# Kernel optimization log

Hardware: AMD Instinct MI355X
Metric: run time of the kernel (lower is better)

Reference implementation:

```python
import jax, jax.numpy as jnp
import numpy as np
import math

W = 256           # one-sided sliding window
G = 64            # number of global tokens (first G positions of every batch row)
HEADS = 8
DMID = 512
HD = DMID // HEADS
B = 2
S = 4096
NEG = jnp.float32(-1e9)   # stands in for the -inf written by mask_invalid_locations (same softmax result)


def setup_inputs() -> dict:
    key = jax.random.key(0)
    ks = jax.random.split(key, 10)
    f = lambda k, sh: jax.random.normal(k, sh, dtype=jnp.float32)
    inp = {
        'hidden_states': f(ks[0], (B, S, DMID)),
        'q': f(ks[1], (S, B, DMID)),
        'k': f(ks[2], (S, B, DMID)),
        'v': f(ks[3], (S, B, DMID)),
        'attn_mask': jnp.broadcast_to((jnp.arange(S) < G).astype(jnp.int32), (B, S)),
    }
    for i, n in enumerate(['q', 'k', 'v', 'qg', 'kg', 'vg']):
        inp['W' + n] = f(ks[4 + i], (DMID, DMID)) * 0.02
        inp['b' + n] = jnp.zeros((DMID,), jnp.float32)
    return inp


def _proj(x, Wt, b):
    # x: (S,B,E) -> (B,S,H,HD)   (matches nn.Linear then view(seq,b,h,hd).transpose(0,1))
    y = x @ Wt.T + b
    return jnp.swapaxes(y.reshape(S, B, HEADS, HD), 0, 1)


def _local_qk(qh, kh):
    # qh, kh: (B,S,H,HD) -> banded scores (B,S,H,2W+1); entry j = key position i + j - W
    C = S // W
    k_pad = jnp.pad(kh, ((0, 0), (W, W), (0, 0), (0, 0)))
    blk = jnp.arange(C)[:, None] * W + jnp.arange(3 * W)[None, :]      # (C,3W) into padded seq
    k_blk = k_pad[:, blk]                                              # (B,C,3W,H,HD)
    q_blk = qh.reshape(B, C, W, HEADS, HD)
    s = jnp.einsum('bcxhd,bcyhd->bcxhy', q_blk, k_blk)                 # (B,C,W,H,3W)
    band = jnp.arange(W)[:, None] + jnp.arange(2 * W + 1)[None, :]     # (W,2W+1): y = x + j
    diag = jnp.take_along_axis(s, band[None, None, :, None, :], axis=-1)
    return diag.reshape(B, S, HEADS, 2 * W + 1)


def _local_pv(p, vh):
    # p: (B,S,H,2W+1) banded probs; vh: (B,S,H,HD) -> (B,S,H,HD)
    C = S // W
    v_pad = jnp.pad(vh, ((0, 0), (W, W), (0, 0), (0, 0)))
    blk = jnp.arange(C)[:, None] * W + jnp.arange(3 * W)[None, :]
    v_blk = v_pad[:, blk]                                              # (B,C,3W,H,HD)
    pc = jnp.moveaxis(p.reshape(B, C, W, HEADS, 2 * W + 1), 3, 2)      # (B,C,H,W,2W+1)
    padded = jnp.pad(pc, ((0, 0), (0, 0), (0, 0), (0, 0), (0, W)))     # (B,C,H,W,3W+1)
    # skew trick: flatten + truncate turns row x shifted by x -> band[x, x+j] = p[x, j]
    full = padded.reshape(B, C, HEADS, W * (3 * W + 1))[..., :W * 3 * W]
    full = full.reshape(B, C, HEADS, W, 3 * W)
    out = jnp.einsum('bchxy,bcyhd->bcxhd', full, v_blk)
    return out.reshape(B, S, HEADS, HD)


def _forward(hidden_states, q, k, v, attn_mask,
             Wq, bq, Wk, bk, Wv, bv, Wqg, bqg, Wkg, bkg, Wvg, bvg):
    scale = 1.0 / math.sqrt(HD)
    qh = _proj(q, Wq, bq) * scale
    kh = _proj(k, Wk, bk)
    vh = _proj(v, Wv, bv)

    local = _local_qk(qh, kh)                                          # (B,S,H,2W+1)
    pos = jnp.arange(S)[:, None] + jnp.arange(2 * W + 1)[None, :] - W  # (S,2W+1) key index
    valid = (pos >= 0) & (pos < S)
    posc = jnp.clip(pos, 0, S - 1)
    # remove_from_windowed_attention_mask: -10000 at nonzero-mask (global/pad) key positions
    fm = jnp.where(attn_mask != 0, jnp.float32(-10000.0), jnp.float32(0.0))  # (B,S)
    dmask = jnp.where(valid[None], fm[:, posc], 0.0)                   # (B,S,2W+1)
    local = jnp.where(valid[None, :, None, :], local, NEG) + dmask[:, :, None, :]

    # every query also attends to the G global keys (concatenated in front)
    sel = jnp.einsum('bshd,bghd->bshg', qh, kh[:, :G])                 # (B,S,H,G)
    scores = jnp.concatenate([sel, local], axis=-1)                    # (B,S,H,G+2W+1)
    probs = jax.nn.softmax(scores, axis=-1)
    kp = attn_mask < 0                                                 # padding queries -> zero rows
    probs = jnp.where(kp[:, :, None, None], 0.0, probs)

    out = jnp.einsum('bshg,bghd->bshd', probs[..., :G], vh[:, :G])
    out = out + _local_pv(probs[..., G:], vh)
    out = out.reshape(B, S, DMID)

    # global-query full attention (W_*_global on hidden_states), overwrites global rows
    qg = ((hidden_states[:, :G] @ Wqg.T + bqg) * scale).reshape(B, G, HEADS, HD)
    kg = (hidden_states @ Wkg.T + bkg).reshape(B, S, HEADS, HD)
    vg = (hidden_states @ Wvg.T + bvg).reshape(B, S, HEADS, HD)
    gw = jnp.einsum('bghd,bshd->bhgs', qg, kg)                         # (B,H,G,S)
    gw = jnp.where(kp[:, None, None, :], jnp.float32(-10000.0), gw)
    gp = jax.nn.softmax(gw, axis=-1)
    gout = jnp.einsum('bhgs,bshd->bghd', gp, vg).reshape(B, G, DMID)
    out = out.at[:, :G, :].set(gout)
    return out


def reference(hidden_states, q, k, v, attn_mask,
              Wq, bq, Wk, bk, Wv, bv, Wqg, bqg, Wkg, bkg, Wvg, bvg):
    return _forward(hidden_states, q, k, v, attn_mask,
                    Wq, bq, Wk, bk, Wv, bv, Wqg, bqg, Wkg, bkg, Wvg, bvg)
```

## Files before the change

### kernel.cpp

```cpp
#include <hip/hip_runtime.h>
#include <cstdint>

#define S_   4096
#define B_   2
#define H_   8
#define HD_  64
#define DM_  512
#define G_   64
#define SEGN 16

typedef __attribute__((ext_vector_type(8))) short bf8_t;
typedef __attribute__((ext_vector_type(4))) float f4_t;
typedef __attribute__((ext_vector_type(4))) unsigned u4_t;
#define MFMA16(A,Bv,C) __builtin_amdgcn_mfma_f32_16x16x32_bf16((A),(Bv),(C),0,0,0)

typedef const unsigned __attribute__((address_space(1)))* gp1_t;
typedef unsigned __attribute__((address_space(3)))* lp3_t;
static __device__ __forceinline__ void gld16(const void* g, void* l){
    __builtin_amdgcn_global_load_lds((gp1_t)g, (lp3_t)l, 16, 0, 0);
}

static __device__ __forceinline__ unsigned short f2bf(float x){
    union { float f; unsigned u; } v; v.f = x;
    unsigned r = v.u + 0x7FFFu + ((v.u >> 16) & 1u);
    return (unsigned short)(r >> 16);
}
static __device__ __forceinline__ unsigned pksplit(float x){
    unsigned u = __float_as_uint(x);
    unsigned t = u & 0xFFFF0000u;
    float r = x - __uint_as_float(t);
    return (u >> 16) | (__float_as_uint(r) & 0xFFFF0000u);
}
static __device__ __forceinline__ float rmax16(float x){
    x=fmaxf(x,__shfl_xor(x,1)); x=fmaxf(x,__shfl_xor(x,2));
    x=fmaxf(x,__shfl_xor(x,4)); x=fmaxf(x,__shfl_xor(x,8)); return x;
}
static __device__ __forceinline__ float rsum16(float x){
    x+=__shfl_xor(x,1); x+=__shfl_xor(x,2); x+=__shfl_xor(x,4); x+=__shfl_xor(x,8); return x;
}

__device__ __forceinline__ int in_row_map(int m, int perm) {
    if (perm == 0) return m;
    if (perm == 1) { int b = m >> 12, s = m & 4095; return s * 2 + b; }
    { int b = m >> 6, g = m & 63; return b * S_ + g; }
}

struct SplitArgs { float* p[4]; };
__global__ __launch_bounds__(256) void split_inplace(SplitArgs a){
    int t = blockIdx.x >> 12;
    int idx = (blockIdx.x & 4095) * 256 + threadIdx.x;
    float* p = a.p[t];
    float4 x = *(const float4*)(p + (size_t)idx * 4);
    unsigned o[4] = { pksplit(x.x), pksplit(x.y), pksplit(x.z), pksplit(x.w) };
    *(u4_t*)(p + (size_t)idx * 4) = *(const u4_t*)o;
}

struct WexpArgs { const float* src[6]; float alpha[6]; unsigned* wa; unsigned* wb; };
__global__ __launch_bounds__(256) void wexpand(WexpArgs a){
    int g = blockIdx.x >> 8;
    int idx = ((blockIdx.x & 255) * 256 + threadIdx.x) * 4;
    const float* s = a.src[g];
    float al = a.alpha[g];
    size_t base = (size_t)g * 262144 + idx;
    float4 x = *(const float4*)(s + idx);
    float xs[4] = { x.x*al, x.y*al, x.z*al, x.w*al };
    unsigned wa4[4], wb4[4];
    #pragma unroll
    for (int j = 0; j < 4; ++j) {
        unsigned u = __float_as_uint(xs[j]);
        unsigned t = u & 0xFFFF0000u;
        float r = xs[j] - __uint_as_float(t);
        unsigned lo = __float_as_uint(r) & 0xFFFF0000u;
        wa4[j] = (u >> 16) | t;
        wb4[j] = (lo >> 16) | lo;
    }
    *(u4_t*)(a.wa + base) = *(const u4_t*)wa4;
    *(u4_t*)(a.wb + base) = *(const u4_t*)wb4;
}

struct ProjDesc {
    const unsigned* A2; const unsigned* Wa; const unsigned* Wb; const float* bias;
    unsigned short* out_r; unsigned short* out_t;
    float balpha; int perm; int mode; int mtiles;
};
struct ProjBatch { ProjDesc d[6]; };

__global__ __launch_bounds__(256) void proj6(ProjBatch pb){
    __shared__ unsigned Asl[128*32];
    __shared__ unsigned Wasl[128*32];
    __shared__ unsigned Wbsl[128*32];
    const ProjDesc d = pb.d[blockIdx.z];
    if ((int)blockIdx.x >= d.mtiles) return;
    const int tid = threadIdx.x;
    const int m0 = blockIdx.x*128, n0 = blockIdx.y*128;
    const int w = tid>>6, l = tid&63, wr = w>>1, wc = w&1, lg = l>>4, lc = l&15;
    const int grow = l>>3, gchk = l&7;

    f4_t acc[4][4];
    #pragma unroll
    for(int i=0;i<4;++i)
        #pragma unroll
        for(int j=0;j<4;++j) acc[i][j] = (f4_t){0.f,0.f,0.f,0.f};

    for (int k0 = 0; k0 < 16; ++k0) {
        __syncthreads();
        #pragma unroll
        for (int t = 0; t < 4; ++t) {
            int row = t*32 + w*8 + grow;
            int sw = (gchk ^ (row & 7)) << 2;
            gld16(d.A2 + (size_t)in_row_map(m0+row, d.perm)*DM_ + k0*32 + sw,
                  (char*)Asl + (t*32 + w*8)*128);
            gld16(d.Wa + (size_t)(n0+row)*DM_ + k0*32 + sw,
                  (char*)Wasl + (t*32 + w*8)*128);
            gld16(d.Wb + (size_t)(n0+row)*DM_ + k0*32 + sw,
                  (char*)Wbsl + (t*32 + w*8)*128);
        }
        __syncthreads();
        #pragma unroll
        for (int ks = 0; ks < 2; ++ks) {
            bf8_t af[4];
            #pragma unroll
            for (int mf = 0; mf < 4; ++mf) {
                int r = wr*64 + mf*16 + lc;
                af[mf] = *(const bf8_t*)((const char*)Asl + r*128 + (((ks*4+lg) ^ (r&7))<<4));
            }
            #pragma unroll
            for (int nf = 0; nf < 4; ++nf) {
                int r = wc*64 + nf*16 + lc;
                int off = r*128 + (((ks*4+lg) ^ (r&7))<<4);
                bf8_t wa = *(const bf8_t*)((const char*)Wasl + off);
                bf8_t wb = *(const bf8_t*)((const char*)Wbsl + off);
                #pragma unroll
                for (int mf = 0; mf < 4; ++mf) {
                    acc[mf][nf] = MFMA16(af[mf], wa, acc[mf][nf]);
                    acc[mf][nf] = MFMA16(af[mf], wb, acc[mf][nf]);
                }
            }
        }
    }
    if (d.mode == 0) {
        #pragma unroll
        for(int nf=0;nf<4;++nf){
            int n = n0 + wc*64 + nf*16 + lc;
            float bv = d.bias[n] * d.balpha;
            #pragma unroll
            for(int mf=0;mf<4;++mf){
                int mb = m0 + wr*64 + mf*16 + lg*4;
                #pragma unroll
                for(int i=0;i<4;++i)
                    d.out_r[(size_t)(mb+i)*DM_ + n] = f2bf(acc[mf][nf][i] + bv);
            }
        }
    } else {
        #pragma unroll
        for(int nf=0;nf<4;++nf){
            int n = n0 + wc*64 + nf*16 + lc;
            int h = n>>6, dl = n&63;
            float bv = d.bias[n];
            #pragma unroll
            for(int mf=0;mf<4;++mf){
                int m = m0 + wr*64 + mf*16 + lg*4;
                int b = m>>12, s = m&4095;
                unsigned short q0=f2bf(acc[mf][nf][0]+bv), q1=f2bf(acc[mf][nf][1]+bv);
                unsigned short q2=f2bf(acc[mf][nf][2]+bv), q3=f2bf(acc[mf][nf][3]+bv);
                unsigned pkw[2] = { (unsigned)q0 | ((unsigned)q1<<16),
                                    (unsigned)q2 | ((unsigned)q3<<16) };
                *(uint2*)(d.out_t + ((size_t)((b*H_+h)*HD_ + dl))*S_ + s) = *(const uint2*)pkw;
            }
        }
    }
}

__global__ __launch_bounds__(256) void attn_fused(
    const unsigned short* __restrict__ Qbf, const unsigned short* __restrict__ Kbf,
    const unsigned short* __restrict__ VT, const unsigned short* __restrict__ QGbf,
    const unsigned short* __restrict__ KGbf, const unsigned short* __restrict__ VGT,
    const int* __restrict__ amask, float* __restrict__ out,
    float* __restrict__ part_m, float* __restrict__ part_l, float* __restrict__ part_o)
{
    __shared__ unsigned short Kls[64*64];
    __shared__ unsigned short Vls[64*64];
    __shared__ unsigned short Ps[64*64];
    const int tid=threadIdx.x, b=blockIdx.z, h=blockIdx.y;
    const int w=tid>>6, l=tid&63, lg=l>>4, lc=l&15;
    const bool is_local = (int)blockIdx.x < 63;
    const int s0 = (blockIdx.x+1)*64;
    const int seg = (int)blockIdx.x - 63;

    const unsigned short* Qsrc = is_local ? (Qbf + ((size_t)(b*S_ + s0 + w*16 + lc))*DM_ + h*HD_)
                                          : (QGbf + ((size_t)(b*G_ + w*16 + lc))*DM_ + h*HD_);
    const unsigned short* Ksrc = is_local ? (Kbf + (size_t)b*S_*DM_ + h*HD_)
                                          : (KGbf + (size_t)b*S_*DM_ + h*HD_);
    const unsigned short* Vsrc = is_local ? (VT + ((size_t)(b*H_+h)*HD_)*S_)
                                          : (VGT + ((size_t)(b*H_+h)*HD_)*S_);

    bf8_t qf[2];
    #pragma unroll
    for(int ks=0;ks<2;++ks) qf[ks] = *(const bf8_t*)(Qsrc + ks*32 + lg*8);

    float m_i[4]={-1e30f,-1e30f,-1e30f,-1e30f}, l_i[4]={0.f,0.f,0.f,0.f};
    f4_t acc_o[4];
    #pragma unroll
    for(int nf=0;nf<4;++nf) acc_o[nf]=(f4_t){0.f,0.f,0.f,0.f};

    const int njc = is_local ? 10 : 4;
    for(int jc=0;jc<njc;++jc){
        const int p0 = is_local ? ((jc==0) ? 0 : (s0-256+(jc-1)*64))
                                : (seg*256 + jc*64);
        if ((unsigned)p0 >= (unsigned)S_) continue;
        {
            const int row0 = w*8 + (l>>3), chk = l&7;
            #pragma unroll
            for (int t = 0; t < 2; ++t) {
                int row = t*32 + row0;
                gld16(Ksrc + (size_t)(p0+row)*DM_ + ((chk ^ (row&7))<<3),
                      (char*)Kls + (t*32 + w*8)*128);
                gld16(Vsrc + (size_t)row*S_ + p0 + ((chk ^ (row&7))<<3),
                      (char*)Vls + (t*32 + w*8)*128);
            }
        }
        __syncthreads();
        f4_t s4[4];
        #pragma unroll
        for(int cf=0;cf<4;++cf) s4[cf]=(f4_t){0.f,0.f,0.f,0.f};
        #pragma unroll
        for(int ks=0;ks<2;++ks)
            #pragma unroll
            for(int cf=0;cf<4;++cf){
                int r = cf*16+lc;
                bf8_t kf = *(const bf8_t*)((const char*)Kls + r*128 + (((ks*4+lg)^(r&7))<<4));
                s4[cf]=MFMA16(qf[ks],kf,s4[cf]);
            }
        if(is_local && jc>0){
            #pragma unroll
            for(int cf=0;cf<4;++cf){
                int p = p0 + cf*16 + lc;
                float madd = (amask[b*S_+p]!=0) ? -10000.f : 0.f;
                #pragma unroll
                for(int i=0;i<4;++i){
                    int rel = p - (s0 + w*16 + lg*4 + i);
                    s4[cf][i] = (rel<-256 || rel>256) ? -1e9f : s4[cf][i]+madd;
                }
            }
        }
        float Pv[4][4];
        #pragma unroll
        for(int i=0;i<4;++i){
            float rm = fmaxf(fmaxf(s4[0][i],s4[1][i]),fmaxf(s4[2][i],s4[3][i]));
            rm = rmax16(rm);
            float mn = fmaxf(m_i[i], rm);
            float rs = 0.f;
            #pragma unroll
            for(int cf=0;cf<4;++cf){ float e=__expf(s4[cf][i]-mn); Pv[cf][i]=e; rs+=e; }
            rs = rsum16(rs);
            float f = __expf(m_i[i]-mn);
            l_i[i] = l_i[i]*f + rs;
            m_i[i] = mn;
            #pragma unroll
            for(int nf=0;nf<4;++nf) acc_o[nf][i]*=f;
        }
        #pragma unroll
        for(int cf=0;cf<4;++cf)
            #pragma unroll
            for(int i=0;i<4;++i){
                int qr = w*16+lg*4+i, p = cf*16+lc;
                Ps[qr*64 + ((((p>>3)^(qr&7))<<3) | (p&7))] = f2bf(Pv[cf][i]);
            }
        __syncthreads();
        #pragma unroll
        for(int ks=0;ks<2;++ks){
            int qr = w*16+lc;
            bf8_t pf = *(const bf8_t*)((const char*)Ps + qr*128 + (((ks*4+lg)^(qr&7))<<4));
            #pragma unroll
            for(int nf=0;nf<4;++nf){
                int dr = nf*16+lc;
                bf8_t vf = *(const bf8_t*)((const char*)Vls + dr*128 + (((ks*4+lg)^(dr&7))<<4));
                acc_o[nf] = MFMA16(pf, vf, acc_o[nf]);
            }
        }
        __syncthreads();
    }
    if (is_local) {
        #pragma unroll
        for(int i=0;i<4;++i){
            float inv = 1.f/l_i[i];
            float* orow = out + ((size_t)(b*S_ + s0 + w*16 + lg*4 + i))*DM_ + h*HD_;
            #pragma unroll
            for(int nf=0;nf<4;++nf) orow[nf*16+lc] = acc_o[nf][i]*inv;
        }
    } else {
        const int pid = (b*H_+h)*SEGN + seg;
        #pragma unroll
        for(int i=0;i<4;++i){
            int qrl = w*16 + lg*4 + i;
            #pragma unroll
            for(int nf=0;nf<4;++nf)
                part_o[(size_t)pid*4096 + qrl*64 + nf*16 + lc] = acc_o[nf][i];
            if(lc==0){
                part_m[pid*64+qrl] = m_i[i];
                part_l[pid*64+qrl] = l_i[i];
            }
        }
    }
}

__global__ __launch_bounds__(256) void global_combine(
    const float* __restrict__ part_m, const float* __restrict__ part_l,
    const float* __restrict__ part_o, float* __restrict__ out)
{
    const int bh = blockIdx.x;
    const int b = bh >> 3, h = bh & 7;
    const int tid = threadIdx.x;
    const int q = tid >> 2, d0 = (tid & 3) * 16;
    float mg = -1e30f;
    for (int s = 0; s < SEGN; ++s)
        mg = fmaxf(mg, part_m[(bh * SEGN + s) * 64 + q]);
    float lsum = 0.f, accv[16] = {};
    for (int s = 0; s < SEGN; ++s) {
        const int pid = bh * SEGN + s;
        float wgt = __expf(part_m[pid * 64 + q] - mg);
        lsum += wgt * part_l[pid * 64 + q];
        const float* op = part_o + (size_t)pid * 4096 + q * 64 + d0;
        #pragma unroll
        for (int t = 0; t < 4; ++t) {
            float tmp[4];
            *(float4*)tmp = *(const float4*)(op + t * 4);
            #pragma unroll
            for (int u = 0; u < 4; ++u) accv[t * 4 + u] += wgt * tmp[u];
        }
    }
    float inv = 1.f / lsum;
    float* orow = out + ((size_t)(b * S_ + q)) * DM_ + h * HD_ + d0;
    #pragma unroll
    for (int t = 0; t < 4; ++t) {
        float o[4];
        #pragma unroll
        for (int u = 0; u < 4; ++u) o[u] = accv[t * 4 + u] * inv;
        *(float4*)(orow + t * 4) = *(const float4*)o;
    }
}

extern "C" void kernel_launch(void* const* d_in, const int* in_sizes, int n_in,
                              void* d_out, int out_size, void* d_ws, size_t ws_size,
                              hipStream_t stream) {
    float* hidden = (float*)d_in[0];
    float* q  = (float*)d_in[1];
    float* k  = (float*)d_in[2];
    float* v  = (float*)d_in[3];
    const int* amask = (const int*)d_in[4];
    const float* Wq  = (const float*)d_in[5];  const float* bq  = (const float*)d_in[6];
    const float* Wk  = (const float*)d_in[7];  const float* bk  = (const float*)d_in[8];
    const float* Wv  = (const float*)d_in[9];  const float* bv  = (const float*)d_in[10];
    const float* Wqg = (const float*)d_in[11]; const float* bqg = (const float*)d_in[12];
    const float* Wkg = (const float*)d_in[13]; const float* bkg = (const float*)d_in[14];
    const float* Wvg = (const float*)d_in[15]; const float* bvg = (const float*)d_in[16];
    float* out = (float*)d_out;

    const size_t NE = (size_t)B_ * S_ * DM_;
    unsigned short* Qbf  = (unsigned short*)d_ws;
    unsigned short* Kbf  = Qbf  + NE;
    unsigned short* VT   = Kbf  + NE;
    unsigned short* KGbf = VT   + NE;
    unsigned short* VGT  = KGbf + NE;
    unsigned short* QGbf = VGT  + NE;
    unsigned* Wa = (unsigned*)(QGbf + (size_t)B_*G_*DM_);
    unsigned* Wb = Wa + 6*262144;
    float* po = (float*)Wa;
    float* pm = (float*)Wb;
    float* pl = pm + B_*H_*SEGN*64;

    dim3 blk(256);
    SplitArgs sa; sa.p[0]=hidden; sa.p[1]=q; sa.p[2]=k; sa.p[3]=v;
    hipLaunchKernelGGL(split_inplace, dim3(4*4096), blk, 0, stream, sa);
    WexpArgs we;
    we.src[0]=Wq; we.src[1]=Wk; we.src[2]=Wv; we.src[3]=Wkg; we.src[4]=Wvg; we.src[5]=Wqg;
    we.alpha[0]=0.125f; we.alpha[1]=1.f; we.alpha[2]=1.f;
    we.alpha[3]=1.f; we.alpha[4]=1.f; we.alpha[5]=0.125f;
    we.wa = Wa; we.wb = Wb;
    hipLaunchKernelGGL(wexpand, dim3(1536), blk, 0, stream, we);

    ProjBatch pp;
    pp.d[0] = { (const unsigned*)q,      Wa + 0*262144, Wb + 0*262144, bq,  Qbf,  nullptr, 0.125f, 1, 0, 64 };
    pp.d[1] = { (const unsigned*)k,      Wa + 1*262144, Wb + 1*262144, bk,  Kbf,  nullptr, 1.0f,   1, 0, 64 };
    pp.d[2] = { (const unsigned*)v,      Wa + 2*262144, Wb + 2*262144, bv,  nullptr, VT,   1.0f,   1, 1, 64 };
    pp.d[3] = { (const unsigned*)hidden, Wa + 3*262144, Wb + 3*262144, bkg, KGbf, nullptr, 1.0f,   0, 0, 64 };
    pp.d[4] = { (const unsigned*)hidden, Wa + 4*262144, Wb + 4*262144, bvg, nullptr, VGT,  1.0f,   0, 1, 64 };
    pp.d[5] = { (const unsigned*)hidden, Wa + 5*262144, Wb + 5*262144, bqg, QGbf, nullptr, 0.125f, 2, 0, 1  };
    hipLaunchKernelGGL(proj6, dim3(64,4,6), blk, 0, stream, pp);

    hipLaunchKernelGGL(attn_fused, dim3(63+SEGN, H_, B_), blk, 0, stream,
                       Qbf, Kbf, VT, QGbf, KGbf, VGT, amask, out, pm, pl, po);

    hipLaunchKernelGGL(global_combine, dim3(B_ * H_), blk, 0, stream, pm, pl, po, out);
}
```

Baseline: 294.8 us.

## Drop weight low-part split, add MFMA priority hints, widen global combine grid

The weight expansion now produces only the high bf16 part of each weight, so the projection GEMM loads one weight tile instead of two and issues half the MFMAs. This removes the hi/lo weight compensation and lowers accuracy of the projections. The change also wraps the MFMA blocks in the projection and attention kernels with s_setprio raises. It splits the global_combine kernel across four times as many blocks, each handling four output elements per thread, to spread the work over more CUs.

```diff
diff --git a/kernel.cpp b/kernel.cpp
--- a/kernel.cpp
+++ b/kernel.cpp
@@ -55,7 +55,7 @@
     *(u4_t*)(p + (size_t)idx * 4) = *(const u4_t*)o;
 }
 
-struct WexpArgs { const float* src[6]; float alpha[6]; unsigned* wa; unsigned* wb; };
+struct WexpArgs { const float* src[6]; float alpha[6]; unsigned* wa; };
 __global__ __launch_bounds__(256) void wexpand(WexpArgs a){
     int g = blockIdx.x >> 8;
     int idx = ((blockIdx.x & 255) * 256 + threadIdx.x) * 4;
@@ -64,22 +64,17 @@
     size_t base = (size_t)g * 262144 + idx;
     float4 x = *(const float4*)(s + idx);
     float xs[4] = { x.x*al, x.y*al, x.z*al, x.w*al };
-    unsigned wa4[4], wb4[4];
+    unsigned wa4[4];
     #pragma unroll
     for (int j = 0; j < 4; ++j) {
         unsigned u = __float_as_uint(xs[j]);
-        unsigned t = u & 0xFFFF0000u;
-        float r = xs[j] - __uint_as_float(t);
-        unsigned lo = __float_as_uint(r) & 0xFFFF0000u;
-        wa4[j] = (u >> 16) | t;
-        wb4[j] = (lo >> 16) | lo;
+        wa4[j] = (u >> 16) | (u & 0xFFFF0000u);
     }
     *(u4_t*)(a.wa + base) = *(const u4_t*)wa4;
-    *(u4_t*)(a.wb + base) = *(const u4_t*)wb4;
 }
 
 struct ProjDesc {
-    const unsigned* A2; const unsigned* Wa; const unsigned* Wb; const float* bias;
+    const unsigned* A2; const unsigned* Wa; const float* bias;
     unsigned short* out_r; unsigned short* out_t;
     float balpha; int perm; int mode; int mtiles;
 };
@@ -88,7 +83,6 @@
 __global__ __launch_bounds__(256) void proj6(ProjBatch pb){
     __shared__ unsigned Asl[128*32];
     __shared__ unsigned Wasl[128*32];
-    __shared__ unsigned Wbsl[128*32];
     const ProjDesc d = pb.d[blockIdx.z];
     if ((int)blockIdx.x >= d.mtiles) return;
     const int tid = threadIdx.x;
@@ -112,13 +106,11 @@
                   (char*)Asl + (t*32 + w*8)*128);
             gld16(d.Wa + (size_t)(n0+row)*DM_ + k0*32 + sw,
                   (char*)Wasl + (t*32 + w*8)*128);
-            gld16(d.Wb + (size_t)(n0+row)*DM_ + k0*32 + sw,
-                  (char*)Wbsl + (t*32 + w*8)*128);
         }
         __syncthreads();
         #pragma unroll
         for (int ks = 0; ks < 2; ++ks) {
-            bf8_t af[4];
+            bf8_t af[4], wf[4];
             #pragma unroll
             for (int mf = 0; mf < 4; ++mf) {
                 int r = wr*64 + mf*16 + lc;
@@ -127,15 +119,15 @@
             #pragma unroll
             for (int nf = 0; nf < 4; ++nf) {
                 int r = wc*64 + nf*16 + lc;
-                int off = r*128 + (((ks*4+lg) ^ (r&7))<<4);
-                bf8_t wa = *(const bf8_t*)((const char*)Wasl + off);
-                bf8_t wb = *(const bf8_t*)((const char*)Wbsl + off);
+                wf[nf] = *(const bf8_t*)((const char*)Wasl + r*128 + (((ks*4+lg) ^ (r&7))<<4));
+            }
+            __builtin_amdgcn_s_setprio(1);
+            #pragma unroll
+            for (int nf = 0; nf < 4; ++nf)
                 #pragma unroll
-                for (int mf = 0; mf < 4; ++mf) {
-                    acc[mf][nf] = MFMA16(af[mf], wa, acc[mf][nf]);
-                    acc[mf][nf] = MFMA16(af[mf], wb, acc[mf][nf]);
-                }
-            }
+                for (int mf = 0; mf < 4; ++mf)
+                    acc[mf][nf] = MFMA16(af[mf], wf[nf], acc[mf][nf]);
+            __builtin_amdgcn_s_setprio(0);
         }
     }
     if (d.mode == 0) {
@@ -223,6 +215,7 @@
         f4_t s4[4];
         #pragma unroll
         for(int cf=0;cf<4;++cf) s4[cf]=(f4_t){0.f,0.f,0.f,0.f};
+        __builtin_amdgcn_s_setprio(1);
         #pragma unroll
         for(int ks=0;ks<2;++ks)
             #pragma unroll
@@ -231,6 +224,7 @@
                 bf8_t kf = *(const bf8_t*)((const char*)Kls + r*128 + (((ks*4+lg)^(r&7))<<4));
                 s4[cf]=MFMA16(qf[ks],kf,s4[cf]);
             }
+        __builtin_amdgcn_s_setprio(0);
         if(is_local && jc>0){
             #pragma unroll
             for(int cf=0;cf<4;++cf){
@@ -267,6 +261,7 @@
                 Ps[qr*64 + ((((p>>3)^(qr&7))<<3) | (p&7))] = f2bf(Pv[cf][i]);
             }
         __syncthreads();
+        __builtin_amdgcn_s_setprio(1);
         #pragma unroll
         for(int ks=0;ks<2;++ks){
             int qr = w*16+lc;
@@ -278,6 +273,7 @@
                 acc_o[nf] = MFMA16(pf, vf, acc_o[nf]);
             }
         }
+        __builtin_amdgcn_s_setprio(0);
         __syncthreads();
     }
     if (is_local) {
@@ -308,36 +304,28 @@
     const float* __restrict__ part_m, const float* __restrict__ part_l,
     const float* __restrict__ part_o, float* __restrict__ out)
 {
-    const int bh = blockIdx.x;
+    const int bh = blockIdx.x >> 2, qq = blockIdx.x & 3;
     const int b = bh >> 3, h = bh & 7;
     const int tid = threadIdx.x;
-    const int q = tid >> 2, d0 = (tid & 3) * 16;
+    const int q = qq * 16 + (tid >> 4), d0 = (tid & 15) * 4;
     float mg = -1e30f;
     for (int s = 0; s < SEGN; ++s)
         mg = fmaxf(mg, part_m[(bh * SEGN + s) * 64 + q]);
-    float lsum = 0.f, accv[16] = {};
+    float lsum = 0.f, accv[4] = {};
     for (int s = 0; s < SEGN; ++s) {
         const int pid = bh * SEGN + s;
         float wgt = __expf(part_m[pid * 64 + q] - mg);
         lsum += wgt * part_l[pid * 64 + q];
-        const float* op = part_o + (size_t)pid * 4096 + q * 64 + d0;
-        #pragma unroll
-        for (int t = 0; t < 4; ++t) {
-            float tmp[4];
-            *(float4*)tmp = *(const float4*)(op + t * 4);
-            #pragma unroll
-            for (int u = 0; u < 4; ++u) accv[t * 4 + u] += wgt * tmp[u];
-        }
+        float tmp[4];
+        *(float4*)tmp = *(const float4*)(part_o + (size_t)pid * 4096 + q * 64 + d0);
+        #pragma unroll
+        for (int u = 0; u < 4; ++u) accv[u] += wgt * tmp[u];
     }
     float inv = 1.f / lsum;
-    float* orow = out + ((size_t)(b * S_ + q)) * DM_ + h * HD_ + d0;
-    #pragma unroll
-    for (int t = 0; t < 4; ++t) {
-        float o[4];
-        #pragma unroll
-        for (int u = 0; u < 4; ++u) o[u] = accv[t * 4 + u] * inv;
-        *(float4*)(orow + t * 4) = *(const float4*)o;
-    }
+    float o[4];
+    #pragma unroll
+    for (int u = 0; u < 4; ++u) o[u] = accv[u] * inv;
+    *(float4*)(out + ((size_t)(b * S_ + q)) * DM_ + h * HD_ + d0) = *(const float4*)o;
 }
 
 extern "C" void kernel_launch(void* const* d_in, const int* in_sizes, int n_in,
@@ -364,9 +352,8 @@
     unsigned short* VGT  = KGbf + NE;
     unsigned short* QGbf = VGT  + NE;
     unsigned* Wa = (unsigned*)(QGbf + (size_t)B_*G_*DM_);
-    unsigned* Wb = Wa + 6*262144;
     float* po = (float*)Wa;
-    float* pm = (float*)Wb;
+    float* pm = (float*)(Wa + 4*262144);
     float* pl = pm + B_*H_*SEGN*64;
 
     dim3 blk(256);
@@ -376,20 +363,20 @@
     we.src[0]=Wq; we.src[1]=Wk; we.src[2]=Wv; we.src[3]=Wkg; we.src[4]=Wvg; we.src[5]=Wqg;
     we.alpha[0]=0.125f; we.alpha[1]=1.f; we.alpha[2]=1.f;
     we.alpha[3]=1.f; we.alpha[4]=1.f; we.alpha[5]=0.125f;
-    we.wa = Wa; we.wb = Wb;
+    we.wa = Wa;
     hipLaunchKernelGGL(wexpand, dim3(1536), blk, 0, stream, we);
 
     ProjBatch pp;
-    pp.d[0] = { (const unsigned*)q,      Wa + 0*262144, Wb + 0*262144, bq,  Qbf,  nullptr, 0.125f, 1, 0, 64 };
-    pp.d[1] = { (const unsigned*)k,      Wa + 1*262144, Wb + 1*262144, bk,  Kbf,  nullptr, 1.0f,   1, 0, 64 };
-    pp.d[2] = { (const unsigned*)v,      Wa + 2*262144, Wb + 2*262144, bv,  nullptr, VT,   1.0f,   1, 1, 64 };
-    pp.d[3] = { (const unsigned*)hidden, Wa + 3*262144, Wb + 3*262144, bkg, KGbf, nullptr, 1.0f,   0, 0, 64 };
-    pp.d[4] = { (const unsigned*)hidden, Wa + 4*262144, Wb + 4*262144, bvg, nullptr, VGT,  1.0f,   0, 1, 64 };
-    pp.d[5] = { (const unsigned*)hidden, Wa + 5*262144, Wb + 5*262144, bqg, QGbf, nullptr, 0.125f, 2, 0, 1  };
+    pp.d[0] = { (const unsigned*)q,      Wa + 0*262144, bq,  Qbf,  nullptr, 0.125f, 1, 0, 64 };
+    pp.d[1] = { (const unsigned*)k,      Wa + 1*262144, bk,  Kbf,  nullptr, 1.0f,   1, 0, 64 };
+    pp.d[2] = { (const unsigned*)v,      Wa + 2*262144, bv,  nullptr, VT,   1.0f,   1, 1, 64 };
+    pp.d[3] = { (const unsigned*)hidden, Wa + 3*262144, bkg, KGbf, nullptr, 1.0f,   0, 0, 64 };
+    pp.d[4] = { (const unsigned*)hidden, Wa + 4*262144, bvg, nullptr, VGT,  1.0f,   0, 1, 64 };
+    pp.d[5] = { (const unsigned*)hidden, Wa + 5*262144, bqg, QGbf, nullptr, 0.125f, 2, 0, 1  };
     hipLaunchKernelGGL(proj6, dim3(64,4,6), blk, 0, stream, pp);
 
     hipLaunchKernelGGL(attn_fused, dim3(63+SEGN, H_, B_), blk, 0, stream,
                        Qbf, Kbf, VT, QGbf, KGbf, VGT, amask, out, pm, pl, po);
 
-    hipLaunchKernelGGL(global_combine, dim3(B_ * H_), blk, 0, stream, pm, pl, po, out);
-}
+    hipLaunchKernelGGL(global_combine, dim3(B_ * H_ * 4), blk, 0, stream, pm, pl, po, out);
+}
```

Measured after the change: 265.8 us. 1.11x faster.
